# Kernel optimization log

Hardware: AMD Instinct MI355X
Metric: run time of the kernel (lower is better)

Reference implementation:

```python
import jax, jax.numpy as jnp
import numpy as np
import math

KEY_SIZE = 128  # init arg; scale = 1/sqrt(key_size)


def setup_inputs() -> dict:
    key = jax.random.key(0)
    kq, kk, kv = jax.random.split(key, 3)
    B, LQ, LK, D, DV = 16, 2048, 2048, 128, 128
    q = jax.random.normal(kq, (B, LQ, D), dtype=jnp.float32)
    k = jax.random.normal(kk, (B, LK, D), dtype=jnp.float32)
    v = jax.random.normal(kv, (B, LK, DV), dtype=jnp.float32)
    return {"q": q, "k": k, "v": v}


def reference(q, k, v):
    scale = 1.0 / math.sqrt(KEY_SIZE)
    # scores: [B, Lq, Lk]
    scores = jnp.einsum('bqd,bkd->bqk', q, k) * scale
    probs = jax.nn.softmax(scores, axis=-1)
    # dropout with p=0.0 is identity (eval-equivalent)
    return jnp.einsum('bqk,bkv->bqv', probs, v)
```

## Files before the change

### kernel.cpp

```cpp
#include <hip/hip_runtime.h>
#include <hip/hip_bf16.h>

typedef float f32x4 __attribute__((ext_vector_type(4)));
typedef short bf16x8 __attribute__((ext_vector_type(8)));

constexpr int NB = 16, LQ = 2048, LK = 2048, D = 128, DV = 128;
constexpr int QBLK = 64, KVBLK = 64, NT = LK / KVBLK;
constexpr float SCALE = 0.08838834764831843f;
constexpr float LOG2E = 1.4426950408889634f;
constexpr float QSCALE = SCALE * LOG2E;

__device__ __forceinline__ unsigned short f2bfs(float f) {
  __hip_bfloat16 h = __float2bfloat16(f);
  return __builtin_bit_cast(unsigned short, h);
}

__device__ __forceinline__ unsigned short f2bf(float f) {
  unsigned int u = __float_as_uint(f);
  u += 0x7FFFu + ((u >> 16) & 1u);
  return (unsigned short)(u >> 16);
}

__device__ __forceinline__ int swz2(int row) {
  return (row ^ (row >> 1) ^ (row >> 3)) & 7;
}

typedef const __attribute__((address_space(1))) void* gas1_t;
typedef __attribute__((address_space(3))) void* las3_t;
__device__ __forceinline__ void gload16(const void* g, void* l) {
  __builtin_amdgcn_global_load_lds((gas1_t)g, (las3_t)l, 16, 0, 0);
}

__global__ __launch_bounds__(256) void conv_bf16(const float* __restrict__ in,
                                                 unsigned short* __restrict__ out,
                                                 float scale) {
  int i = blockIdx.x * 256 + threadIdx.x;
  f32x4 a = ((const f32x4*)in)[2 * i];
  f32x4 b = ((const f32x4*)in)[2 * i + 1];
  bf16x8 r;
  #pragma unroll
  for (int j = 0; j < 4; ++j) {
    r[j]     = (short)f2bfs(a[j] * scale);
    r[4 + j] = (short)f2bfs(b[j] * scale);
  }
  ((bf16x8*)out)[i] = r;
}

__global__ __launch_bounds__(256) void conv_vt(const float* __restrict__ v,
                                               unsigned short* __restrict__ vt) {
  __shared__ __align__(16) unsigned short tb[64 * 64];
  const int tid = threadIdx.x;
  const int k0 = blockIdx.x * 64, dv0 = blockIdx.y * 64, b = blockIdx.z;
  {
    const int kk = tid >> 2, dd0 = (tid & 3) * 16;
    const float* src = v + ((long)(b * LK + k0 + kk)) * DV + dv0 + dd0;
    f32x4 a0 = ((const f32x4*)src)[0];
    f32x4 a1 = ((const f32x4*)src)[1];
    f32x4 a2 = ((const f32x4*)src)[2];
    f32x4 a3 = ((const f32x4*)src)[3];
    bf16x8 r0, r1;
    #pragma unroll
    for (int j = 0; j < 4; ++j) {
      r0[j] = (short)f2bfs(a0[j]); r0[4 + j] = (short)f2bfs(a1[j]);
      r1[j] = (short)f2bfs(a2[j]); r1[4 + j] = (short)f2bfs(a3[j]);
    }
    int ch = dd0 >> 3;
    *(bf16x8*)&tb[kk * 64 + ((ch ^ swz2(kk)) << 3)] = r0;
    *(bf16x8*)&tb[kk * 64 + (((ch + 1) ^ swz2(kk)) << 3)] = r1;
  }
  __syncthreads();
  {
    const int dv = tid >> 2, ks = (tid & 3) * 16;
    bf16x8 w0, w1;
    #pragma unroll
    for (int j = 0; j < 8; ++j) {
      int r0 = ks + j, r1 = ks + 8 + j;
      w0[j] = (short)tb[r0 * 64 + (((dv >> 3) ^ swz2(r0)) << 3) + (dv & 7)];
      w1[j] = (short)tb[r1 * 64 + (((dv >> 3) ^ swz2(r1)) << 3) + (dv & 7)];
    }
    unsigned short* dst = vt + ((long)(b * DV + dv0 + dv)) * LK + k0 + ks;
    *(bf16x8*)dst = w0;
    *(bf16x8*)(dst + 8) = w1;
  }
}

__global__ __launch_bounds__(256, 2) void attn_fwd2(
    const float* __restrict__ qp, const unsigned short* __restrict__ wsK,
    const unsigned short* __restrict__ wsVt, float* __restrict__ op) {
  __shared__ __align__(16) unsigned short sm[32768];

  const int tid = threadIdx.x;
  const int wid = tid >> 6;
  const int lane = tid & 63;
  const int g = lane >> 4;
  const int c = lane & 15;

  const int bid = blockIdx.x;
  const int sbid = (bid & 7) * 64 + (bid >> 3);
  const int b = sbid >> 5;
  const int qb = (sbid & 31) * QBLK;

  const float* qrow = qp + ((long)(b * LQ + qb + wid * 16 + c)) * D;
  bf16x8 aq[4];
  #pragma unroll
  for (int ks = 0; ks < 4; ++ks) {
    f32x4 x0 = *(const f32x4*)(qrow + ks * 32 + g * 8);
    f32x4 x1 = *(const f32x4*)(qrow + ks * 32 + g * 8 + 4);
    #pragma unroll
    for (int j = 0; j < 4; ++j) {
      aq[ks][j]     = (short)f2bfs(x0[j] * QSCALE);
      aq[ks][4 + j] = (short)f2bfs(x1[j] * QSCALE);
    }
  }

  const unsigned short* kbatch = wsK + (long)b * LK * D;
  const unsigned short* vbatch = wsVt + (long)b * DV * LK;

  auto stage = [&](int buf, int kv0) {
    const unsigned short* ksrc = kbatch + (long)kv0 * D;
    #pragma unroll
    for (int it = 0; it < 4; ++it) {
      int ci = it * 256 + tid, row = ci >> 4, c16 = ci & 15;
      gload16(ksrc + row * D + ((c16 ^ swz2(row)) << 3), &sm[buf * 16384 + ci * 8]);
    }
    #pragma unroll
    for (int it = 0; it < 4; ++it) {
      int ci = it * 256 + tid, row = ci >> 3, c8 = ci & 7;
      gload16(vbatch + (long)row * LK + kv0 + ((c8 ^ swz2(row)) << 3),
              &sm[buf * 16384 + 8192 + ci * 8]);
    }
  };

  stage(0, 0);
  __syncthreads();

  f32x4 o[8];
  f32x4 fz = {0.f, 0.f, 0.f, 0.f};
  #pragma unroll
  for (int i = 0; i < 8; ++i) o[i] = fz;
  float m_s = -1e30f, l_s = 0.f;

  for (int t = 0; t < NT; ++t) {
    const int cur = t & 1;
    if (t + 1 < NT) stage(cur ^ 1, (t + 1) * KVBLK);
    const int kb = cur * 16384, vb = kb + 8192;

    f32x4 s[4];
    #pragma unroll
    for (int i = 0; i < 4; ++i) s[i] = fz;
    __builtin_amdgcn_s_setprio(1);
    #pragma unroll
    for (int tt = 0; tt < 4; ++tt) {
      int row = 32 * (tt >> 1) + 4 * (tt & 1) + (c & 3) + ((c >> 2) << 3);
      int sz = swz2(row);
      #pragma unroll
      for (int ks = 0; ks < 4; ++ks) {
        bf16x8 ak = *(const bf16x8*)&sm[kb + row * 128 + ((((ks << 2) + g) ^ sz) << 3)];
        s[tt] = __builtin_amdgcn_mfma_f32_16x16x32_bf16(ak, aq[ks], s[tt], 0, 0, 0);
      }
    }
    __builtin_amdgcn_s_setprio(0);

    float pm = s[0][0];
    #pragma unroll
    for (int tt = 0; tt < 4; ++tt)
      #pragma unroll
      for (int r = 0; r < 4; ++r) pm = fmaxf(pm, s[tt][r]);
    pm = fmaxf(pm, __shfl_xor(pm, 16));
    pm = fmaxf(pm, __shfl_xor(pm, 32));
    if (!__all(pm <= m_s + 8.0f)) {
      float mn = fmaxf(m_s, pm);
      float al = exp2f(m_s - mn);
      l_s *= al;
      float al4[4];
      #pragma unroll
      for (int r = 0; r < 4; ++r) al4[r] = __shfl(al, 4 * g + r);
      #pragma unroll
      for (int dvt = 0; dvt < 8; ++dvt)
        #pragma unroll
        for (int r = 0; r < 4; ++r) o[dvt][r] *= al4[r];
      m_s = mn;
    }
    float sum = 0.f;
    #pragma unroll
    for (int tt = 0; tt < 4; ++tt)
      #pragma unroll
      for (int r = 0; r < 4; ++r) {
        float p = exp2f(s[tt][r] - m_s);
        s[tt][r] = p;
        sum += p;
      }
    sum += __shfl_xor(sum, 16);
    sum += __shfl_xor(sum, 32);
    l_s += sum;

    bf16x8 pa[2];
    #pragma unroll
    for (int ks = 0; ks < 2; ++ks) {
      #pragma unroll
      for (int j = 0; j < 4; ++j) {
        pa[ks][j]     = (short)f2bfs(s[2 * ks][j]);
        pa[ks][4 + j] = (short)f2bfs(s[2 * ks + 1][j]);
      }
    }

    __builtin_amdgcn_s_setprio(1);
    #pragma unroll
    for (int ks = 0; ks < 2; ++ks) {
      #pragma unroll
      for (int dvt = 0; dvt < 8; ++dvt) {
        int row = dvt * 16 + c;
        bf16x8 vbf = *(const bf16x8*)&sm[vb + row * 64 + ((((ks << 2) + g) ^ swz2(row)) << 3)];
        o[dvt] = __builtin_amdgcn_mfma_f32_16x16x32_bf16(pa[ks], vbf, o[dvt], 0, 0, 0);
      }
    }
    __builtin_amdgcn_s_setprio(0);

    __syncthreads();
  }

  float linv[4];
  #pragma unroll
  for (int r = 0; r < 4; ++r) linv[r] = 1.f / __shfl(l_s, 4 * g + r);
  float* dst = op + ((long)(b * LQ + qb + wid * 16)) * DV;
  #pragma unroll
  for (int r = 0; r < 4; ++r)
    #pragma unroll
    for (int dvt = 0; dvt < 8; ++dvt)
      dst[(4 * g + r) * DV + dvt * 16 + c] = o[dvt][r] * linv[r];
}

__device__ __forceinline__ int swzc(int row, int c16) {
  return c16 ^ ((row ^ (row >> 3)) & 7);
}

__global__ __launch_bounds__(256, 2) void attn_fwd(
    const float* __restrict__ qp, const float* __restrict__ kp,
    const float* __restrict__ vp, float* __restrict__ op) {
  __shared__ __align__(16) unsigned short smm[28672];
  const int tid = threadIdx.x, wid = tid >> 6, lane = tid & 63;
  const int g = lane >> 4, c = lane & 15;
  const int b = blockIdx.y, qb = blockIdx.x * QBLK;
  const float* qg = qp + ((long)b * LQ + qb) * D;
  const float* kg = kp + (long)b * LK * D;
  const float* vg = vp + (long)b * LK * DV;
  #pragma unroll
  for (int it = 0; it < 4; ++it) {
    int ch = it * 256 + tid, row = ch >> 4, c16 = ch & 15;
    const float* src = qg + row * D + c16 * 8;
    f32x4 f0 = *(const f32x4*)(src);
    f32x4 f1 = *(const f32x4*)(src + 4);
    bf16x8 fr;
    #pragma unroll
    for (int j = 0; j < 4; ++j) {
      fr[j] = (short)f2bf(f0[j] * SCALE);
      fr[4 + j] = (short)f2bf(f1[j] * SCALE);
    }
    *(bf16x8*)&smm[row * 128 + swzc(row, c16) * 8] = fr;
  }
  __syncthreads();
  bf16x8 aq[4];
  #pragma unroll
  for (int ks = 0; ks < 4; ++ks) {
    int row = wid * 16 + c;
    aq[ks] = *(const bf16x8*)&smm[row * 128 + swzc(row, ks * 4 + g) * 8];
  }
  f32x4 o[8]; f32x4 fz = {0.f, 0.f, 0.f, 0.f};
  #pragma unroll
  for (int i = 0; i < 8; ++i) o[i] = fz;
  float m_r[4] = {-1e30f, -1e30f, -1e30f, -1e30f};
  float l_r[4] = {0.f, 0.f, 0.f, 0.f};
  const int pbase = 24576 + wid * 1024;
  for (int kv0 = 0; kv0 < LK; kv0 += KVBLK) {
    __syncthreads();
    const float* ksrc = kg + (long)kv0 * D;
    #pragma unroll
    for (int it = 0; it < 4; ++it) {
      int ch = it * 256 + tid, row = ch >> 4, c16 = ch & 15;
      const float* src = ksrc + row * D + c16 * 8;
      f32x4 f0 = *(const f32x4*)(src);
      f32x4 f1 = *(const f32x4*)(src + 4);
      bf16x8 fr;
      #pragma unroll
      for (int j = 0; j < 4; ++j) { fr[j] = (short)f2bf(f0[j]); fr[4 + j] = (short)f2bf(f1[j]); }
      *(bf16x8*)&smm[8192 + row * 128 + swzc(row, c16) * 8] = fr;
    }
    {
      const float* vsrc = vg + (long)kv0 * DV;
      int dvq = (tid & 31) * 4, kg8 = tid >> 5;
      f32x4 col[8];
      #pragma unroll
      for (int j = 0; j < 8; ++j) col[j] = *(const f32x4*)(vsrc + (kg8 * 8 + j) * DV + dvq);
      #pragma unroll
      for (int i = 0; i < 4; ++i) {
        int dv = dvq + i;
        bf16x8 fr;
        #pragma unroll
        for (int j = 0; j < 8; ++j) fr[j] = (short)f2bf(col[j][i]);
        *(bf16x8*)&smm[16384 + dv * 64 + swzc(dv, kg8) * 8] = fr;
      }
    }
    __syncthreads();
    f32x4 s[4];
    #pragma unroll
    for (int i = 0; i < 4; ++i) s[i] = fz;
    #pragma unroll
    for (int ks = 0; ks < 4; ++ks) {
      #pragma unroll
      for (int t = 0; t < 4; ++t) {
        int row = t * 16 + c;
        bf16x8 bk = *(const bf16x8*)&smm[8192 + row * 128 + swzc(row, ks * 4 + g) * 8];
        s[t] = __builtin_amdgcn_mfma_f32_16x16x32_bf16(aq[ks], bk, s[t], 0, 0, 0);
      }
    }
    #pragma unroll
    for (int r = 0; r < 4; ++r) {
      float pm = fmaxf(fmaxf(s[0][r], s[1][r]), fmaxf(s[2][r], s[3][r]));
      pm = fmaxf(pm, __shfl_xor(pm, 1));
      pm = fmaxf(pm, __shfl_xor(pm, 2));
      pm = fmaxf(pm, __shfl_xor(pm, 4));
      pm = fmaxf(pm, __shfl_xor(pm, 8));
      float mn = fmaxf(m_r[r], pm);
      float al = exp2f((m_r[r] - mn) * LOG2E);
      float sum = 0.f;
      #pragma unroll
      for (int t = 0; t < 4; ++t) {
        float p = exp2f((s[t][r] - mn) * LOG2E);
        s[t][r] = p; sum += p;
      }
      sum += __shfl_xor(sum, 1); sum += __shfl_xor(sum, 2);
      sum += __shfl_xor(sum, 4); sum += __shfl_xor(sum, 8);
      l_r[r] = l_r[r] * al + sum; m_r[r] = mn;
      #pragma unroll
      for (int dvt = 0; dvt < 8; ++dvt) o[dvt][r] *= al;
    }
    #pragma unroll
    for (int t = 0; t < 4; ++t)
      #pragma unroll
      for (int r = 0; r < 4; ++r) {
        int row = g * 4 + r, colx = c + 16 * t;
        smm[pbase + row * 64 + swzc(row, colx >> 3) * 8 + (colx & 7)] = f2bf(s[t][r]);
      }
    #pragma unroll
    for (int ks = 0; ks < 2; ++ks) {
      bf16x8 pa = *(const bf16x8*)&smm[pbase + c * 64 + swzc(c, ks * 4 + g) * 8];
      #pragma unroll
      for (int dvt = 0; dvt < 8; ++dvt) {
        int row = dvt * 16 + c;
        bf16x8 vb2 = *(const bf16x8*)&smm[16384 + row * 64 + swzc(row, ks * 4 + g) * 8];
        o[dvt] = __builtin_amdgcn_mfma_f32_16x16x32_bf16(pa, vb2, o[dvt], 0, 0, 0);
      }
    }
  }
  float* dst = op + ((long)b * LQ + qb + wid * 16) * DV;
  #pragma unroll
  for (int r = 0; r < 4; ++r) {
    float inv = 1.f / l_r[r];
    #pragma unroll
    for (int dvt = 0; dvt < 8; ++dvt)
      dst[(g * 4 + r) * DV + dvt * 16 + c] = o[dvt][r] * inv;
  }
}

extern "C" void kernel_launch(void* const* d_in, const int* in_sizes, int n_in,
                              void* d_out, int out_size, void* d_ws, size_t ws_size,
                              hipStream_t stream) {
  const float* q = (const float*)d_in[0];
  const float* k = (const float*)d_in[1];
  const float* v = (const float*)d_in[2];
  float* out = (float*)d_out;

  const size_t kelems = (size_t)NB * LK * D;
  const size_t need = kelems * 2 * 2;
  if (ws_size >= need) {
    unsigned short* wsK = (unsigned short*)d_ws;
    unsigned short* wsVt = wsK + kelems;
    conv_bf16<<<dim3((int)(kelems / 8 / 256)), dim3(256), 0, stream>>>(k, wsK, 1.0f);
    conv_vt<<<dim3(LK / 64, DV / 64, NB), dim3(256), 0, stream>>>(v, wsVt);
    attn_fwd2<<<dim3(NB * LQ / QBLK), dim3(256), 0, stream>>>(q, wsK, wsVt, out);
  } else {
    attn_fwd<<<dim3(LQ / QBLK, NB), dim3(256), 0, stream>>>(q, k, v, out);
  }
}
```

Measured before the change: 80.65 us.

## Process two 16-row query tiles per wave to double K/V LDS reuse

Each wave now owns 32 query rows (two 16-row tiles) instead of 16, so each workgroup covers 128 query rows and the grid is halved. Every K and V fragment read from LDS feeds two MFMAs, which halves LDS traffic and global K/V staging per unit of output. The cost is double the accumulator and score registers (o, s, aq), which may strain the 2-waves-per-SIMD launch bound and cause spills. The block count also drops to 256, which could leave some compute units underused.

Measured after the change: 89.67 us. +11.2%, slower.

```diff
diff --git a/kernel.cpp b/kernel.cpp
--- a/kernel.cpp
+++ b/kernel.cpp
@@ -5,7 +5,7 @@
 typedef short bf16x8 __attribute__((ext_vector_type(8)));
 
 constexpr int NB = 16, LQ = 2048, LK = 2048, D = 128, DV = 128;
-constexpr int QBLK = 64, KVBLK = 64, NT = LK / KVBLK;
+constexpr int KVBLK = 64, NT = LK / KVBLK;
 constexpr float SCALE = 0.08838834764831843f;
 constexpr float LOG2E = 1.4426950408889634f;
 constexpr float QSCALE = SCALE * LOG2E;
@@ -84,7 +84,7 @@
   }
 }
 
-__global__ __launch_bounds__(256, 2) void attn_fwd2(
+__global__ __launch_bounds__(256, 2) void attn_fwd3(
     const float* __restrict__ qp, const unsigned short* __restrict__ wsK,
     const unsigned short* __restrict__ wsVt, float* __restrict__ op) {
   __shared__ __align__(16) unsigned short sm[32768];
@@ -96,20 +96,24 @@
   const int c = lane & 15;
 
   const int bid = blockIdx.x;
-  const int sbid = (bid & 7) * 64 + (bid >> 3);
-  const int b = sbid >> 5;
-  const int qb = (sbid & 31) * QBLK;
-
-  const float* qrow = qp + ((long)(b * LQ + qb + wid * 16 + c)) * D;
-  bf16x8 aq[4];
-  #pragma unroll
-  for (int ks = 0; ks < 4; ++ks) {
-    f32x4 x0 = *(const f32x4*)(qrow + ks * 32 + g * 8);
-    f32x4 x1 = *(const f32x4*)(qrow + ks * 32 + g * 8 + 4);
-    #pragma unroll
-    for (int j = 0; j < 4; ++j) {
-      aq[ks][j]     = (short)f2bfs(x0[j] * QSCALE);
-      aq[ks][4 + j] = (short)f2bfs(x1[j] * QSCALE);
+  const int sbid = (bid & 7) * 32 + (bid >> 3);
+  const int b = sbid >> 4;
+  const int qb = (sbid & 15) * 128;
+  const int qwave = qb + wid * 32;
+
+  bf16x8 aq[2][4];
+  #pragma unroll
+  for (int h = 0; h < 2; ++h) {
+    const float* qrow = qp + ((long)(b * LQ + qwave + h * 16 + c)) * D;
+    #pragma unroll
+    for (int ks = 0; ks < 4; ++ks) {
+      f32x4 x0 = *(const f32x4*)(qrow + ks * 32 + g * 8);
+      f32x4 x1 = *(const f32x4*)(qrow + ks * 32 + g * 8 + 4);
+      #pragma unroll
+      for (int j = 0; j < 4; ++j) {
+        aq[h][ks][j]     = (short)f2bfs(x0[j] * QSCALE);
+        aq[h][ks][4 + j] = (short)f2bfs(x1[j] * QSCALE);
+      }
     }
   }
 
@@ -134,20 +138,25 @@
   stage(0, 0);
   __syncthreads();
 
-  f32x4 o[8];
+  f32x4 o[2][8];
   f32x4 fz = {0.f, 0.f, 0.f, 0.f};
   #pragma unroll
-  for (int i = 0; i < 8; ++i) o[i] = fz;
-  float m_s = -1e30f, l_s = 0.f;
+  for (int h = 0; h < 2; ++h)
+    #pragma unroll
+    for (int i = 0; i < 8; ++i) o[h][i] = fz;
+  float m_s[2] = {-1e30f, -1e30f};
+  float l_s[2] = {0.f, 0.f};
 
   for (int t = 0; t < NT; ++t) {
     const int cur = t & 1;
     if (t + 1 < NT) stage(cur ^ 1, (t + 1) * KVBLK);
     const int kb = cur * 16384, vb = kb + 8192;
 
-    f32x4 s[4];
-    #pragma unroll
-    for (int i = 0; i < 4; ++i) s[i] = fz;
+    f32x4 s[2][4];
+    #pragma unroll
+    for (int h = 0; h < 2; ++h)
+      #pragma unroll
+      for (int i = 0; i < 4; ++i) s[h][i] = fz;
     __builtin_amdgcn_s_setprio(1);
     #pragma unroll
     for (int tt = 0; tt < 4; ++tt) {
@@ -156,51 +165,55 @@
       #pragma unroll
       for (int ks = 0; ks < 4; ++ks) {
         bf16x8 ak = *(const bf16x8*)&sm[kb + row * 128 + ((((ks << 2) + g) ^ sz) << 3)];
-        s[tt] = __builtin_amdgcn_mfma_f32_16x16x32_bf16(ak, aq[ks], s[tt], 0, 0, 0);
+        s[0][tt] = __builtin_amdgcn_mfma_f32_16x16x32_bf16(ak, aq[0][ks], s[0][tt], 0, 0, 0);
+        s[1][tt] = __builtin_amdgcn_mfma_f32_16x16x32_bf16(ak, aq[1][ks], s[1][tt], 0, 0, 0);
       }
     }
     __builtin_amdgcn_s_setprio(0);
 
-    float pm = s[0][0];
-    #pragma unroll
-    for (int tt = 0; tt < 4; ++tt)
-      #pragma unroll
-      for (int r = 0; r < 4; ++r) pm = fmaxf(pm, s[tt][r]);
-    pm = fmaxf(pm, __shfl_xor(pm, 16));
-    pm = fmaxf(pm, __shfl_xor(pm, 32));
-    if (!__all(pm <= m_s + 8.0f)) {
-      float mn = fmaxf(m_s, pm);
-      float al = exp2f(m_s - mn);
-      l_s *= al;
-      float al4[4];
-      #pragma unroll
-      for (int r = 0; r < 4; ++r) al4[r] = __shfl(al, 4 * g + r);
-      #pragma unroll
-      for (int dvt = 0; dvt < 8; ++dvt)
-        #pragma unroll
-        for (int r = 0; r < 4; ++r) o[dvt][r] *= al4[r];
-      m_s = mn;
-    }
-    float sum = 0.f;
-    #pragma unroll
-    for (int tt = 0; tt < 4; ++tt)
-      #pragma unroll
-      for (int r = 0; r < 4; ++r) {
-        float p = exp2f(s[tt][r] - m_s);
-        s[tt][r] = p;
-        sum += p;
-      }
-    sum += __shfl_xor(sum, 16);
-    sum += __shfl_xor(sum, 32);
-    l_s += sum;
-
-    bf16x8 pa[2];
-    #pragma unroll
-    for (int ks = 0; ks < 2; ++ks) {
-      #pragma unroll
-      for (int j = 0; j < 4; ++j) {
-        pa[ks][j]     = (short)f2bfs(s[2 * ks][j]);
-        pa[ks][4 + j] = (short)f2bfs(s[2 * ks + 1][j]);
+    bf16x8 pa[2][2];
+    #pragma unroll
+    for (int h = 0; h < 2; ++h) {
+      float pm = s[h][0][0];
+      #pragma unroll
+      for (int tt = 0; tt < 4; ++tt)
+        #pragma unroll
+        for (int r = 0; r < 4; ++r) pm = fmaxf(pm, s[h][tt][r]);
+      pm = fmaxf(pm, __shfl_xor(pm, 16));
+      pm = fmaxf(pm, __shfl_xor(pm, 32));
+      if (!__all(pm <= m_s[h] + 8.0f)) {
+        float mn = fmaxf(m_s[h], pm);
+        float al = exp2f(m_s[h] - mn);
+        l_s[h] *= al;
+        float al4[4];
+        #pragma unroll
+        for (int r = 0; r < 4; ++r) al4[r] = __shfl(al, 4 * g + r);
+        #pragma unroll
+        for (int dvt = 0; dvt < 8; ++dvt)
+          #pragma unroll
+          for (int r = 0; r < 4; ++r) o[h][dvt][r] *= al4[r];
+        m_s[h] = mn;
+      }
+      float sum = 0.f;
+      #pragma unroll
+      for (int tt = 0; tt < 4; ++tt)
+        #pragma unroll
+        for (int r = 0; r < 4; ++r) {
+          float p = exp2f(s[h][tt][r] - m_s[h]);
+          s[h][tt][r] = p;
+          sum += p;
+        }
+      sum += __shfl_xor(sum, 16);
+      sum += __shfl_xor(sum, 32);
+      l_s[h] += sum;
+
+      #pragma unroll
+      for (int ks = 0; ks < 2; ++ks) {
+        #pragma unroll
+        for (int j = 0; j < 4; ++j) {
+          pa[h][ks][j]     = (short)f2bfs(s[h][2 * ks][j]);
+          pa[h][ks][4 + j] = (short)f2bfs(s[h][2 * ks + 1][j]);
+        }
       }
     }
 
@@ -211,7 +224,8 @@
       for (int dvt = 0; dvt < 8; ++dvt) {
         int row = dvt * 16 + c;
         bf16x8 vbf = *(const bf16x8*)&sm[vb + row * 64 + ((((ks << 2) + g) ^ swz2(row)) << 3)];
-        o[dvt] = __builtin_amdgcn_mfma_f32_16x16x32_bf16(pa[ks], vbf, o[dvt], 0, 0, 0);
+        o[0][dvt] = __builtin_amdgcn_mfma_f32_16x16x32_bf16(pa[0][ks], vbf, o[0][dvt], 0, 0, 0);
+        o[1][dvt] = __builtin_amdgcn_mfma_f32_16x16x32_bf16(pa[1][ks], vbf, o[1][dvt], 0, 0, 0);
       }
     }
     __builtin_amdgcn_s_setprio(0);
@@ -219,15 +233,18 @@
     __syncthreads();
   }
 
-  float linv[4];
-  #pragma unroll
-  for (int r = 0; r < 4; ++r) linv[r] = 1.f / __shfl(l_s, 4 * g + r);
-  float* dst = op + ((long)(b * LQ + qb + wid * 16)) * DV;
-  #pragma unroll
-  for (int r = 0; r < 4; ++r)
-    #pragma unroll
-    for (int dvt = 0; dvt < 8; ++dvt)
-      dst[(4 * g + r) * DV + dvt * 16 + c] = o[dvt][r] * linv[r];
+  #pragma unroll
+  for (int h = 0; h < 2; ++h) {
+    float linv[4];
+    #pragma unroll
+    for (int r = 0; r < 4; ++r) linv[r] = 1.f / __shfl(l_s[h], 4 * g + r);
+    float* dst = op + ((long)(b * LQ + qwave + h * 16)) * DV;
+    #pragma unroll
+    for (int r = 0; r < 4; ++r)
+      #pragma unroll
+      for (int dvt = 0; dvt < 8; ++dvt)
+        dst[(4 * g + r) * DV + dvt * 16 + c] = o[h][dvt][r] * linv[r];
+  }
 }
 
 __device__ __forceinline__ int swzc(int row, int c16) {
@@ -240,7 +257,7 @@
   __shared__ __align__(16) unsigned short smm[28672];
   const int tid = threadIdx.x, wid = tid >> 6, lane = tid & 63;
   const int g = lane >> 4, c = lane & 15;
-  const int b = blockIdx.y, qb = blockIdx.x * QBLK;
+  const int b = blockIdx.y, qb = blockIdx.x * 64;
   const float* qg = qp + ((long)b * LQ + qb) * D;
   const float* kg = kp + (long)b * LK * D;
   const float* vg = vp + (long)b * LK * DV;
@@ -377,8 +394,8 @@
     unsigned short* wsVt = wsK + kelems;
     conv_bf16<<<dim3((int)(kelems / 8 / 256)), dim3(256), 0, stream>>>(k, wsK, 1.0f);
     conv_vt<<<dim3(LK / 64, DV / 64, NB), dim3(256), 0, stream>>>(v, wsVt);
-    attn_fwd2<<<dim3(NB * LQ / QBLK), dim3(256), 0, stream>>>(q, wsK, wsVt, out);
+    attn_fwd3<<<dim3(NB * LQ / 128), dim3(256), 0, stream>>>(q, wsK, wsVt, out);
   } else {
-    attn_fwd<<<dim3(LQ / QBLK, NB), dim3(256), 0, stream>>>(q, k, v, out);
-  }
-}
+    attn_fwd<<<dim3(LQ / 64, NB), dim3(256), 0, stream>>>(q, k, v, out);
+  }
+}
```
